# Kernel tuning notes

Hardware: AMD Instinct MI355X
Metric: run time of the kernel (lower is better)

The kernel has to match this reference:

```python
import jax, jax.numpy as jnp
import numpy as np
from jax import lax

POST_NMS_TOP_N = 1000   # cfg[cfg_key].RPN_POST_NMS_TOP_N
NMS_THRESH = 0.7        # cfg[cfg_key].RPN_NMS_THRESH
NEG = -1e9
B, N = 4, 65536


def setup_inputs() -> dict:
    key = jax.random.key(0)
    k0, k1, k2, k3, k4, k5, k6 = jax.random.split(key, 7)
    scores = jax.random.uniform(k0, (B, N), dtype=jnp.float32)
    # small deltas so exp(dw) stays in a realistic range
    bbox_deltas = 0.1 * jax.random.normal(k1, (B, N, 4), dtype=jnp.float32)
    # plausible anchor boxes inside a 1024x1024 image
    cx = jax.random.uniform(k2, (N,), minval=0.0, maxval=1024.0)
    cy = jax.random.uniform(k3, (N,), minval=0.0, maxval=1024.0)
    w = jax.random.uniform(k4, (N,), minval=16.0, maxval=256.0)
    h = jax.random.uniform(k5, (N,), minval=16.0, maxval=256.0)
    anchors = jnp.stack([cx - 0.5 * w, cy - 0.5 * h, cx + 0.5 * w, cy + 0.5 * h], axis=-1).astype(jnp.float32)
    im_info = jnp.tile(jnp.array([[1024.0, 1024.0, 1.0]], dtype=jnp.float32), (B, 1))
    ids = jax.random.randint(k6, (N,), 0, 5, dtype=jnp.int32)  # FPN level ids
    return {"scores": scores, "bbox_deltas": bbox_deltas, "anchors": anchors,
            "im_info": im_info, "ids": ids}


def _iou_one(box, boxes):
    # box [4], boxes [N,4]; mmcv convention (no +1)
    x1 = jnp.maximum(box[0], boxes[:, 0])
    y1 = jnp.maximum(box[1], boxes[:, 1])
    x2 = jnp.minimum(box[2], boxes[:, 2])
    y2 = jnp.minimum(box[3], boxes[:, 3])
    inter = jnp.clip(x2 - x1, 0.0) * jnp.clip(y2 - y1, 0.0)
    a1 = (box[2] - box[0]) * (box[3] - box[1])
    a2 = (boxes[:, 2] - boxes[:, 0]) * (boxes[:, 3] - boxes[:, 1])
    return inter / jnp.maximum(a1 + a2 - inter, 1e-6)


def _nms_single(boxes, scores, ids):
    # batched_nms: offset boxes by level id so levels never suppress each other
    max_c = jnp.max(boxes) + 1.0
    boxes_off = boxes + (ids.astype(boxes.dtype) * max_c)[:, None]

    def step(s, _):
        i = jnp.argmax(s)
        valid = s[i] > NEG * 0.5
        iou = _iou_one(boxes_off[i], boxes_off)
        s_new = jnp.where(iou > NMS_THRESH, NEG, s).at[i].set(NEG)
        sel = jnp.where(valid, boxes[i], jnp.zeros((4,), boxes.dtype))
        return s_new, sel

    _, sel = lax.scan(step, scores, None, length=POST_NMS_TOP_N)
    return sel  # [POST_NMS_TOP_N, 4], in descending score order (as batched_nms returns)


def _forward(scores, bbox_deltas, anchors, im_info, ids):
    ws = anchors[:, 2] - anchors[:, 0] + 1.0          # [N]
    hs = anchors[:, 3] - anchors[:, 1] + 1.0
    ctr_x = anchors[:, 0] + 0.5 * ws
    ctr_y = anchors[:, 1] + 0.5 * hs
    dx, dy, dw, dh = (bbox_deltas[..., 0], bbox_deltas[..., 1],
                      bbox_deltas[..., 2], bbox_deltas[..., 3])  # [B,N]
    pcx = dx * ws + ctr_x
    pcy = dy * hs + ctr_y
    pw = jnp.exp(dw) * ws
    ph = jnp.exp(dh) * hs
    proposals = jnp.stack([pcx - 0.5 * pw, pcy - 0.5 * ph,
                           pcx + 0.5 * pw, pcy + 0.5 * ph], axis=-1)  # [B,N,4]
    # clip_boxes: x in [0, w-1], y in [0, h-1]
    wmax = im_info[:, 1][:, None] - 1.0
    hmax = im_info[:, 0][:, None] - 1.0
    x1 = jnp.clip(proposals[..., 0], 0.0, wmax)
    y1 = jnp.clip(proposals[..., 1], 0.0, hmax)
    x2 = jnp.clip(proposals[..., 2], 0.0, wmax)
    y2 = jnp.clip(proposals[..., 3], 0.0, hmax)
    proposals = jnp.stack([x1, y1, x2, y2], axis=-1)
    # per-image batched NMS (greedy descending-score selection == sort + NMS)
    sel = jax.vmap(_nms_single, in_axes=(0, 0, None))(proposals, scores, ids)  # [B,topN,4]
    batch_col = jnp.broadcast_to(
        jnp.arange(scores.shape[0], dtype=sel.dtype)[:, None, None],
        (scores.shape[0], POST_NMS_TOP_N, 1))
    return jnp.concatenate([batch_col, sel], axis=-1)  # [B,topN,5]


def reference(scores, bbox_deltas, anchors, im_info, ids):
    return _forward(scores, bbox_deltas, anchors, im_info, ids)
```

## Files before the change

kernel.cpp:

```cpp
#include <hip/hip_runtime.h>
#include <stdint.h>

#define NB     65536
#define BATCH  4
#define TOPN   1000
#define MMAX   2048
#define NTILE  (MMAX / 64)
#define NPAIRS (NTILE * (NTILE + 1) / 2)
#define CAP    128
#define KSUP   8
#define UNC    128
#define THRESH 0.974f
#define NEGV   (-1e9f)
#define NMS_T  0.7f

#define OFF_CBLK   64
#define OFF_MBLK   1088
#define OFF_KRAW   2112
#define OFF_SBOX   264256
#define OFF_SLEV   395328
#define OFF_CNT2   428096
#define OFF_SUP    460864

__device__ __forceinline__ void decode_box(const float4* __restrict__ anchors4,
                                           const float4* __restrict__ deltas4,
                                           int b, int i, float wmax, float hmax,
                                           float& x1, float& y1, float& x2, float& y2) {
  float4 a = anchors4[i];
  float4 d = deltas4[(size_t)b * NB + i];
  float ws = a.z - a.x + 1.0f;
  float hs = a.w - a.y + 1.0f;
  float cx = a.x + 0.5f * ws;
  float cy = a.y + 0.5f * hs;
  float pcx = d.x * ws + cx;
  float pcy = d.y * hs + cy;
  float pw = expf(d.z) * ws;
  float ph = expf(d.w) * hs;
  x1 = pcx - 0.5f * pw; y1 = pcy - 0.5f * ph;
  x2 = pcx + 0.5f * pw; y2 = pcy + 0.5f * ph;
  x1 = fminf(fmaxf(x1, 0.0f), wmax);
  y1 = fminf(fmaxf(y1, 0.0f), hmax);
  x2 = fminf(fmaxf(x2, 0.0f), wmax);
  y2 = fminf(fmaxf(y2, 0.0f), hmax);
}

__device__ __forceinline__ uint32_t blockscan(uint32_t v, volatile uint32_t* wsum,
                                              int tid, uint32_t* total) {
  __syncthreads();
  int lane = tid & 63, wid = tid >> 6;
  uint32_t x = v;
  for (int off = 1; off < 64; off <<= 1) {
    uint32_t u = __shfl_up(x, off, 64);
    if (lane >= off) x += u;
  }
  if (lane == 63) wsum[wid] = x;
  __syncthreads();
  if (tid == 0) {
    uint32_t run = 0;
    for (int w = 0; w < 4; ++w) { uint32_t t = wsum[w]; wsum[w] = run; run += t; }
    wsum[4] = run;
  }
  __syncthreads();
  *total = wsum[4];
  return x - v + wsum[wid];
}

__global__ __launch_bounds__(256) void k_prep(const float* __restrict__ scores,
                                              const float4* __restrict__ deltas4,
                                              const float4* __restrict__ anchors4,
                                              const float* __restrict__ im_info,
                                              unsigned long long* __restrict__ keys_raw,
                                              uint32_t* __restrict__ cnt_blk,
                                              uint32_t* __restrict__ maxc_blk) {
  const int b = blockIdx.x >> 6;
  const int blk = blockIdx.x & 63;
  const int tid = threadIdx.x;
  const int lane = tid & 63, wid = tid >> 6;
  __shared__ uint32_t wsum[5];
  __shared__ float fred[4];
  const float wmax = im_info[b * 3 + 1] - 1.0f;
  const float hmax = im_info[b * 3 + 0] - 1.0f;
  float sc4[4];
  uint32_t cmask = 0, ccount = 0;
  float mcoord = 0.0f;
#pragma unroll
  for (int k = 0; k < 4; ++k) {
    int i = (blk << 10) + (k << 8) + tid;
    float x1, y1, x2, y2;
    decode_box(anchors4, deltas4, b, i, wmax, hmax, x1, y1, x2, y2);
    mcoord = fmaxf(mcoord, fmaxf(fmaxf(x1, y1), fmaxf(x2, y2)));
    float sc = scores[(size_t)b * NB + i];
    sc4[k] = sc;
    if (sc >= THRESH) { cmask |= (1u << k); ccount++; }
  }
  for (int o = 32; o > 0; o >>= 1) mcoord = fmaxf(mcoord, __shfl_xor(mcoord, o, 64));
  if (lane == 0) fred[wid] = mcoord;
  uint32_t total;
  uint32_t ebase = blockscan(ccount, wsum, tid, &total);
  if (tid == 0) {
    cnt_blk[blockIdx.x] = total;
    maxc_blk[blockIdx.x] =
        __float_as_uint(fmaxf(fmaxf(fred[0], fred[1]), fmaxf(fred[2], fred[3])));
  }
  uint32_t p = ebase;
  unsigned long long* dst = keys_raw + (size_t)blockIdx.x * CAP;
#pragma unroll
  for (int k = 0; k < 4; ++k) {
    if (cmask & (1u << k)) {
      if (p < (uint32_t)CAP) {
        int i = (blk << 10) + (k << 8) + tid;
        dst[p] = ((unsigned long long)(~__float_as_uint(sc4[k])) << 32) | (uint32_t)i;
      }
      p++;
    }
  }
}

__global__ __launch_bounds__(256) void k_rank(const uint32_t* __restrict__ cnt_blk,
                                              const uint32_t* __restrict__ maxc_blk,
                                              const unsigned long long* __restrict__ keys_raw,
                                              const float4* __restrict__ deltas4,
                                              const float4* __restrict__ anchors4,
                                              const float* __restrict__ im_info,
                                              const int* __restrict__ ids,
                                              uint32_t* ctrs,
                                              float4* sboxes, int* slev,
                                              uint32_t* cnt2) {
  const int b = blockIdx.y;
  const int r = blockIdx.x;
  const int tid = threadIdx.x;
  const int lane = tid & 63, wid = tid >> 6;
  __shared__ unsigned long long sk[MMAX];
  __shared__ uint32_t scnt[64], sbs[64];
  __shared__ uint32_t psum[256];
  __shared__ uint32_t meta[3];

  if (tid < 64) {
    uint32_t c = cnt_blk[b * 64 + tid];
    uint32_t cc = min(c, (uint32_t)CAP);
    uint32_t mb = maxc_blk[b * 64 + tid];
    scnt[tid] = cc;
    uint32_t x = cc;
    for (int off = 1; off < 64; off <<= 1) {
      uint32_t u = __shfl_up(x, off, 64);
      if (lane >= off) x += u;
    }
    sbs[tid] = x - cc;
    for (int off = 32; off > 0; off >>= 1)
      mb = max(mb, (uint32_t)__shfl_xor((int)mb, off, 64));
    unsigned long long ov = __ballot(c > (uint32_t)CAP);
    if (tid == 63) { meta[0] = x; meta[2] = (ov != 0ULL) ? 1u : 0u; }
    if (tid == 0) meta[1] = mb;
  }
  __syncthreads();
  uint32_t nsum = meta[0];
  int n = min((int)nsum, MMAX);
  uint32_t flag = meta[2] | ((nsum > (uint32_t)MMAX) ? 1u : 0u);
  if (r == 0 && tid == 0) {
    ctrs[b] = (uint32_t)n;
    ctrs[4 + b] = meta[1];
    ctrs[8 + b] = flag;
  }
  if (tid < 64) cnt2[(size_t)b * MMAX + r * 64 + tid] = 0u;
  {
    int k = tid >> 2, q = tid & 3;
    uint32_t cb = sbs[k], cc = scnt[k];
    const unsigned long long* src = keys_raw + ((size_t)b * 64 + k) * CAP;
    for (uint32_t o = q; o < cc; o += 4) {
      uint32_t d = cb + o;
      if (d < (uint32_t)MMAX) sk[d] = src[o];
    }
  }
  for (int i = tid; i < MMAX; i += 256) if (i >= n) sk[i] = ~0ULL;
  __syncthreads();
  int c = r * 64 + lane;
  uint32_t partial = 0;
  if (c < n) {
    unsigned long long myk = sk[c];
    const ulonglong2* p2 = (const ulonglong2*)(sk + (size_t)wid * 512);
    for (int it = 0; it < 256; it += 4) {
      ulonglong2 a = p2[it], bq = p2[it + 1], cq = p2[it + 2], dq = p2[it + 3];
      partial += (uint32_t)(a.x < myk) + (uint32_t)(a.y < myk) +
                 (uint32_t)(bq.x < myk) + (uint32_t)(bq.y < myk) +
                 (uint32_t)(cq.x < myk) + (uint32_t)(cq.y < myk) +
                 (uint32_t)(dq.x < myk) + (uint32_t)(dq.y < myk);
    }
  }
  psum[wid * 64 + lane] = partial;
  __syncthreads();
  if (tid < 64) {
    int cc = r * 64 + tid;
    if (cc < n) {
      uint32_t rank = psum[tid] + psum[64 + tid] + psum[128 + tid] + psum[192 + tid];
      if (rank < (uint32_t)MMAX) {
        unsigned long long key = sk[cc];
        int i = (int)(uint32_t)key;
        float wmax = im_info[b * 3 + 1] - 1.0f;
        float hmax = im_info[b * 3 + 0] - 1.0f;
        float x1, y1, x2, y2;
        decode_box(anchors4, deltas4, b, i, wmax, hmax, x1, y1, x2, y2);
        sboxes[(size_t)b * MMAX + rank] = make_float4(x1, y1, x2, y2);
        slev[(size_t)b * MMAX + rank] = ids[i];
      }
    }
  }
}

__global__ __launch_bounds__(64) void k_pairs(uint32_t* ctrs,
                                              const float4* __restrict__ sboxes,
                                              const int* __restrict__ slev,
                                              uint32_t* cnt2, int* suplist) {
  int b = blockIdx.y;
  int p = blockIdx.x;
  int tj = (int)((sqrtf(8.0f * (float)p + 1.0f) - 1.0f) * 0.5f);
  while ((tj + 1) * (tj + 2) / 2 <= p) ++tj;
  while (tj * (tj + 1) / 2 > p) --tj;
  int ti = p - tj * (tj + 1) / 2;
  int n = min((int)ctrs[b], MMAX);
  if (tj * 64 >= n) return;
  float max_c = __uint_as_float(ctrs[4 + b]) + 1.0f;
  int lane = threadIdx.x;

  __shared__ float4 ib[64];
  __shared__ int il[64];
  int ii = ti * 64 + lane;
  if (ii < n) {
    float4 v = sboxes[(size_t)b * MMAX + ii];
    int lv = slev[(size_t)b * MMAX + ii];
    float off = (float)lv * max_c;
    ib[lane] = make_float4(v.x + off, v.y + off, v.z + off, v.w + off);
    il[lane] = lv;
  } else {
    il[lane] = -1;
  }
  int j = tj * 64 + lane;
  float4 J = make_float4(0.f, 0.f, 0.f, 0.f);
  int jl = -2;
  float aj = 0.0f;
  if (j < n) {
    float4 v = sboxes[(size_t)b * MMAX + j];
    jl = slev[(size_t)b * MMAX + j];
    float off = (float)jl * max_c;
    J = make_float4(v.x + off, v.y + off, v.z + off, v.w + off);
    aj = (J.z - J.x) * (J.w - J.y);
  }
  __syncthreads();
  if (j < n) {
    int imax = (ti == tj) ? lane : 64;
    for (int k = 0; k < imax; ++k) {
      if (il[k] != jl) continue;
      float4 I = ib[k];
      float xx1 = fmaxf(I.x, J.x), yy1 = fmaxf(I.y, J.y);
      float xx2 = fminf(I.z, J.z), yy2 = fminf(I.w, J.w);
      float inter = fmaxf(xx2 - xx1, 0.0f) * fmaxf(yy2 - yy1, 0.0f);
      float ai = (I.z - I.x) * (I.w - I.y);
      float iou = inter / fmaxf((ai + aj) - inter, 1e-6f);
      if (iou > NMS_T) {
        uint32_t s = atomicAdd(&cnt2[(size_t)b * MMAX + j], 1u);
        if (s < (uint32_t)KSUP) suplist[((size_t)b * MMAX + j) * KSUP + s] = ti * 64 + k;
        else ctrs[8 + b] = 1u;
      }
    }
  }
}

__device__ __forceinline__ uint32_t scan_pair(uint32_t pairsum, volatile uint32_t* wsum,
                                              int tid, uint32_t* total_out) {
  int lane = tid & 63, wid = tid >> 6;
  uint32_t v = pairsum;
  for (int off = 1; off < 64; off <<= 1) {
    uint32_t u = __shfl_up(v, off, 64);
    if (lane >= off) v += u;
  }
  if (lane == 63) wsum[wid] = v;
  __syncthreads();
  if (tid == 0) {
    uint32_t run = 0;
    for (int w = 0; w < 16; ++w) { uint32_t t = wsum[w]; wsum[w] = run; run += t; }
    wsum[16] = run;
  }
  __syncthreads();
  uint32_t incl = v + wsum[wid];
  *total_out = wsum[16];
  return incl - pairsum;
}

__global__ __launch_bounds__(1024) void k_resolve(uint32_t* ctrs,
                                                  const uint32_t* __restrict__ cnt2,
                                                  const int* __restrict__ suplist,
                                                  const float4* __restrict__ sboxes,
                                                  float* __restrict__ out) {
  int b = blockIdx.x;
  int tid = threadIdx.x;
  __shared__ uint8_t kept[MMAX];
  __shared__ uint32_t wsum[17];
  __shared__ uint16_t unc[UNC];
  __shared__ int supld[UNC][KSUP];
  __shared__ uint8_t supn[UNC];
  int n = min((int)ctrs[b], MMAX);
  int j0 = tid * 2, j1 = tid * 2 + 1;
  uint32_t c0 = (j0 < n) ? cnt2[(size_t)b * MMAX + j0] : 0u;
  uint32_t c1 = (j1 < n) ? cnt2[(size_t)b * MMAX + j1] : 0u;
  kept[j0] = (j0 < n && c0 == 0u) ? 1 : 0;
  kept[j1] = (j1 < n && c1 == 0u) ? 1 : 0;
  uint32_t u0 = (j0 < n && c0 > 0u) ? 1u : 0u;
  uint32_t u1 = (j1 < n && c1 > 0u) ? 1u : 0u;
  uint32_t tot_unc;
  uint32_t base = scan_pair(u0 + u1, wsum, tid, &tot_unc);
  if (u0) {
    uint32_t p = base;
    if (p < UNC) {
      int m = (int)min(c0, (uint32_t)KSUP);
      unc[p] = (uint16_t)j0; supn[p] = (uint8_t)m;
      for (int s = 0; s < m; ++s) supld[p][s] = suplist[((size_t)b * MMAX + j0) * KSUP + s];
    }
  }
  if (u1) {
    uint32_t p = base + u0;
    if (p < UNC) {
      int m = (int)min(c1, (uint32_t)KSUP);
      unc[p] = (uint16_t)j1; supn[p] = (uint8_t)m;
      for (int s = 0; s < m; ++s) supld[p][s] = suplist[((size_t)b * MMAX + j1) * KSUP + s];
    }
  }
  __syncthreads();
  if (tid < 64) {
    int nu = (int)min(tot_unc, (uint32_t)UNC);
    for (int u = 0; u < nu; ++u) {
      int m = (int)supn[u];
      int pred = (tid < m) ? (int)kept[supld[u][tid]] : 0;
      unsigned long long bal = __ballot(pred);
      if (tid == 0) kept[unc[u]] = (bal == 0ULL) ? 1 : 0;
    }
  }
  __syncthreads();
  uint32_t k0 = kept[j0], k1 = kept[j1];
  uint32_t total;
  uint32_t pbase = scan_pair(k0 + k1, wsum, tid, &total);
  if (k0 && pbase < (uint32_t)TOPN) {
    float4 bx = sboxes[(size_t)b * MMAX + j0];
    size_t o = ((size_t)b * TOPN + pbase) * 5;
    out[o] = (float)b; out[o+1] = bx.x; out[o+2] = bx.y; out[o+3] = bx.z; out[o+4] = bx.w;
  }
  if (k1) {
    uint32_t p = pbase + k0;
    if (p < (uint32_t)TOPN) {
      float4 bx = sboxes[(size_t)b * MMAX + j1];
      size_t o = ((size_t)b * TOPN + p) * 5;
      out[o] = (float)b; out[o+1] = bx.x; out[o+2] = bx.y; out[o+3] = bx.z; out[o+4] = bx.w;
    }
  }
  for (int t = tid; t < TOPN; t += 1024) {
    if ((uint32_t)t >= total) {
      size_t o = ((size_t)b * TOPN + t) * 5;
      out[o] = (float)b; out[o+1] = 0.0f; out[o+2] = 0.0f; out[o+3] = 0.0f; out[o+4] = 0.0f;
    }
  }
  if (tid == 0 && (total < (uint32_t)TOPN || tot_unc > (uint32_t)UNC)) ctrs[8 + b] = 1u;
}

__global__ __launch_bounds__(1024) void k_fallback(const float* __restrict__ scores,
                                                   const float4* __restrict__ deltas4,
                                                   const float4* __restrict__ anchors4,
                                                   const float* __restrict__ im_info,
                                                   const int* __restrict__ ids,
                                                   const uint32_t* __restrict__ ctrs,
                                                   float* __restrict__ out) {
  int b = blockIdx.x;
  if (ctrs[8 + b] == 0u) return;
  int tid = threadIdx.x;
  __shared__ uint32_t mask[NB / 32];
  __shared__ float rv[1024];
  __shared__ int ri[1024];
  float max_c = __uint_as_float(ctrs[4 + b]) + 1.0f;
  float wmax = im_info[b * 3 + 1] - 1.0f;
  float hmax = im_info[b * 3 + 0] - 1.0f;
  for (int i = tid; i < NB / 32; i += 1024) mask[i] = 0u;
  __syncthreads();
  for (int it = 0; it < TOPN; ++it) {
    float bv = -3e38f; int bi = 0x7fffffff;
    for (int i = tid; i < NB; i += 1024) {
      bool sup = (mask[i >> 5] >> (i & 31)) & 1u;
      float v = sup ? NEGV : scores[(size_t)b * NB + i];
      if (v > bv || (v == bv && i < bi)) { bv = v; bi = i; }
    }
    rv[tid] = bv; ri[tid] = bi;
    __syncthreads();
    for (int s = 512; s > 0; s >>= 1) {
      if (tid < s) {
        float v2 = rv[tid + s]; int i2 = ri[tid + s];
        if (v2 > rv[tid] || (v2 == rv[tid] && i2 < ri[tid])) { rv[tid] = v2; ri[tid] = i2; }
      }
      __syncthreads();
    }
    int ii = ri[0]; float vv = rv[0];
    bool valid = vv > NEGV * 0.5f;
    if (!valid) {
      if (tid == 0) {
        size_t o = ((size_t)b * TOPN + it) * 5;
        out[o] = (float)b; out[o+1] = 0; out[o+2] = 0; out[o+3] = 0; out[o+4] = 0;
      }
      __syncthreads();
      continue;
    }
    float x1, y1, x2, y2;
    decode_box(anchors4, deltas4, b, ii, wmax, hmax, x1, y1, x2, y2);
    int lv = ids[ii];
    float off = (float)lv * max_c;
    float s0 = x1 + off, s1 = y1 + off, s2 = x2 + off, s3 = y2 + off;
    float a1 = (s2 - s0) * (s3 - s1);
    if (tid == 0) {
      size_t o = ((size_t)b * TOPN + it) * 5;
      out[o] = (float)b; out[o+1] = x1; out[o+2] = y1; out[o+3] = x2; out[o+4] = y2;
    }
    for (int j = tid; j < NB; j += 1024) {
      if ((mask[j >> 5] >> (j & 31)) & 1u) continue;
      if (ids[j] != lv) continue;
      float bx1, by1, bx2, by2;
      decode_box(anchors4, deltas4, b, j, wmax, hmax, bx1, by1, bx2, by2);
      float t0 = bx1 + off, t1 = by1 + off, t2 = bx2 + off, t3 = by2 + off;
      float xx1 = fmaxf(s0, t0), yy1 = fmaxf(s1, t1);
      float xx2 = fminf(s2, t2), yy2 = fminf(s3, t3);
      float inter = fmaxf(xx2 - xx1, 0.0f) * fmaxf(yy2 - yy1, 0.0f);
      float a2r = (t2 - t0) * (t3 - t1);
      float iou = inter / fmaxf(a1 + a2r - inter, 1e-6f);
      if (iou > NMS_T) atomicOr(&mask[j >> 5], 1u << (j & 31));
    }
    if (tid == 0) atomicOr(&mask[ii >> 5], 1u << (ii & 31));
    __syncthreads();
  }
}

extern "C" void kernel_launch(void* const* d_in, const int* in_sizes, int n_in,
                              void* d_out, int out_size, void* d_ws, size_t ws_size,
                              hipStream_t stream) {
  const float*  scores   = (const float*)d_in[0];
  const float4* deltas4  = (const float4*)d_in[1];
  const float4* anchors4 = (const float4*)d_in[2];
  const float*  im_info  = (const float*)d_in[3];
  const int*    ids      = (const int*)d_in[4];
  float* out = (float*)d_out;

  char* ws = (char*)d_ws;
  uint32_t*           ctrs     = (uint32_t*)ws;
  uint32_t*           cnt_blk  = (uint32_t*)(ws + OFF_CBLK);
  uint32_t*           maxc_blk = (uint32_t*)(ws + OFF_MBLK);
  unsigned long long* keys_raw = (unsigned long long*)(ws + OFF_KRAW);
  float4*             sboxes   = (float4*)(ws + OFF_SBOX);
  int*                slev     = (int*)(ws + OFF_SLEV);
  uint32_t*           cnt2     = (uint32_t*)(ws + OFF_CNT2);
  int*                suplist  = (int*)(ws + OFF_SUP);

  hipLaunchKernelGGL(k_prep, dim3(64 * BATCH), dim3(256), 0, stream,
                     scores, deltas4, anchors4, im_info, keys_raw, cnt_blk, maxc_blk);
  hipLaunchKernelGGL(k_rank, dim3(NTILE, BATCH), dim3(256), 0, stream,
                     cnt_blk, maxc_blk, keys_raw, deltas4, anchors4, im_info, ids,
                     ctrs, sboxes, slev, cnt2);
  hipLaunchKernelGGL(k_pairs, dim3(NPAIRS, BATCH), dim3(64), 0, stream,
                     ctrs, sboxes, slev, cnt2, suplist);
  hipLaunchKernelGGL(k_resolve, dim3(BATCH), dim3(1024), 0, stream,
                     ctrs, cnt2, suplist, sboxes, out);
  hipLaunchKernelGGL(k_fallback, dim3(BATCH), dim3(1024), 0, stream,
                     scores, deltas4, anchors4, im_info, ids, ctrs, out);
}
```

Baseline: 102.7 us.

## Drop full-box decode from prep and fold fallback into output kernel

The prep kernel now reads only scores, as float4 loads, to build candidate keys. It no longer decodes every anchor box just to find the maximum coordinate, which avoids streaming all deltas and anchors on the common path. Level separation in the pair kernel now relies on the level-id comparison instead of coordinate offsets, so the global max coordinate is only needed by the exact fallback, which computes it lazily. The resolve and fallback kernels are merged into one, removing a launch; the merged kernel carries a larger shared-memory footprint and does an extra decode pass when the fallback fires.

```diff
diff --git a/kernel.cpp b/kernel.cpp
--- a/kernel.cpp
+++ b/kernel.cpp
@@ -15,12 +15,11 @@
 #define NMS_T  0.7f
 
 #define OFF_CBLK   64
-#define OFF_MBLK   1088
-#define OFF_KRAW   2112
-#define OFF_SBOX   264256
-#define OFF_SLEV   395328
-#define OFF_CNT2   428096
-#define OFF_SUP    460864
+#define OFF_KRAW   1088
+#define OFF_SBOX   263232
+#define OFF_SLEV   394304
+#define OFF_CNT2   427072
+#define OFF_SUP    459840
 
 __device__ __forceinline__ void decode_box(const float4* __restrict__ anchors4,
                                            const float4* __restrict__ deltas4,
@@ -66,49 +65,28 @@
 }
 
 __global__ __launch_bounds__(256) void k_prep(const float* __restrict__ scores,
-                                              const float4* __restrict__ deltas4,
-                                              const float4* __restrict__ anchors4,
-                                              const float* __restrict__ im_info,
                                               unsigned long long* __restrict__ keys_raw,
-                                              uint32_t* __restrict__ cnt_blk,
-                                              uint32_t* __restrict__ maxc_blk) {
+                                              uint32_t* __restrict__ cnt_blk) {
   const int b = blockIdx.x >> 6;
   const int blk = blockIdx.x & 63;
   const int tid = threadIdx.x;
-  const int lane = tid & 63, wid = tid >> 6;
   __shared__ uint32_t wsum[5];
-  __shared__ float fred[4];
-  const float wmax = im_info[b * 3 + 1] - 1.0f;
-  const float hmax = im_info[b * 3 + 0] - 1.0f;
-  float sc4[4];
+  const float4* s4 = (const float4*)scores + (size_t)b * (NB / 4) + (size_t)blk * 256 + tid;
+  float4 s = *s4;
+  float sc4[4] = {s.x, s.y, s.z, s.w};
   uint32_t cmask = 0, ccount = 0;
-  float mcoord = 0.0f;
 #pragma unroll
-  for (int k = 0; k < 4; ++k) {
-    int i = (blk << 10) + (k << 8) + tid;
-    float x1, y1, x2, y2;
-    decode_box(anchors4, deltas4, b, i, wmax, hmax, x1, y1, x2, y2);
-    mcoord = fmaxf(mcoord, fmaxf(fmaxf(x1, y1), fmaxf(x2, y2)));
-    float sc = scores[(size_t)b * NB + i];
-    sc4[k] = sc;
-    if (sc >= THRESH) { cmask |= (1u << k); ccount++; }
-  }
-  for (int o = 32; o > 0; o >>= 1) mcoord = fmaxf(mcoord, __shfl_xor(mcoord, o, 64));
-  if (lane == 0) fred[wid] = mcoord;
+  for (int k = 0; k < 4; ++k)
+    if (sc4[k] >= THRESH) { cmask |= (1u << k); ccount++; }
   uint32_t total;
-  uint32_t ebase = blockscan(ccount, wsum, tid, &total);
-  if (tid == 0) {
-    cnt_blk[blockIdx.x] = total;
-    maxc_blk[blockIdx.x] =
-        __float_as_uint(fmaxf(fmaxf(fred[0], fred[1]), fmaxf(fred[2], fred[3])));
-  }
-  uint32_t p = ebase;
+  uint32_t p = blockscan(ccount, wsum, tid, &total);
+  if (tid == 0) cnt_blk[blockIdx.x] = total;
   unsigned long long* dst = keys_raw + (size_t)blockIdx.x * CAP;
 #pragma unroll
   for (int k = 0; k < 4; ++k) {
     if (cmask & (1u << k)) {
       if (p < (uint32_t)CAP) {
-        int i = (blk << 10) + (k << 8) + tid;
+        int i = (blk << 10) + (tid << 2) + k;
         dst[p] = ((unsigned long long)(~__float_as_uint(sc4[k])) << 32) | (uint32_t)i;
       }
       p++;
@@ -117,7 +95,6 @@
 }
 
 __global__ __launch_bounds__(256) void k_rank(const uint32_t* __restrict__ cnt_blk,
-                                              const uint32_t* __restrict__ maxc_blk,
                                               const unsigned long long* __restrict__ keys_raw,
                                               const float4* __restrict__ deltas4,
                                               const float4* __restrict__ anchors4,
@@ -133,12 +110,11 @@
   __shared__ unsigned long long sk[MMAX];
   __shared__ uint32_t scnt[64], sbs[64];
   __shared__ uint32_t psum[256];
-  __shared__ uint32_t meta[3];
+  __shared__ uint32_t meta[2];
 
   if (tid < 64) {
     uint32_t c = cnt_blk[b * 64 + tid];
     uint32_t cc = min(c, (uint32_t)CAP);
-    uint32_t mb = maxc_blk[b * 64 + tid];
     scnt[tid] = cc;
     uint32_t x = cc;
     for (int off = 1; off < 64; off <<= 1) {
@@ -146,19 +122,15 @@
       if (lane >= off) x += u;
     }
     sbs[tid] = x - cc;
-    for (int off = 32; off > 0; off >>= 1)
-      mb = max(mb, (uint32_t)__shfl_xor((int)mb, off, 64));
     unsigned long long ov = __ballot(c > (uint32_t)CAP);
-    if (tid == 63) { meta[0] = x; meta[2] = (ov != 0ULL) ? 1u : 0u; }
-    if (tid == 0) meta[1] = mb;
+    if (tid == 63) { meta[0] = x; meta[1] = (ov != 0ULL) ? 1u : 0u; }
   }
   __syncthreads();
   uint32_t nsum = meta[0];
   int n = min((int)nsum, MMAX);
-  uint32_t flag = meta[2] | ((nsum > (uint32_t)MMAX) ? 1u : 0u);
+  uint32_t flag = meta[1] | ((nsum > (uint32_t)MMAX) ? 1u : 0u);
   if (r == 0 && tid == 0) {
     ctrs[b] = (uint32_t)n;
-    ctrs[4 + b] = meta[1];
     ctrs[8 + b] = flag;
   }
   if (tid < 64) cnt2[(size_t)b * MMAX + r * 64 + tid] = 0u;
@@ -218,18 +190,14 @@
   int ti = p - tj * (tj + 1) / 2;
   int n = min((int)ctrs[b], MMAX);
   if (tj * 64 >= n) return;
-  float max_c = __uint_as_float(ctrs[4 + b]) + 1.0f;
   int lane = threadIdx.x;
 
   __shared__ float4 ib[64];
   __shared__ int il[64];
   int ii = ti * 64 + lane;
   if (ii < n) {
-    float4 v = sboxes[(size_t)b * MMAX + ii];
-    int lv = slev[(size_t)b * MMAX + ii];
-    float off = (float)lv * max_c;
-    ib[lane] = make_float4(v.x + off, v.y + off, v.z + off, v.w + off);
-    il[lane] = lv;
+    ib[lane] = sboxes[(size_t)b * MMAX + ii];
+    il[lane] = slev[(size_t)b * MMAX + ii];
   } else {
     il[lane] = -1;
   }
@@ -238,10 +206,8 @@
   int jl = -2;
   float aj = 0.0f;
   if (j < n) {
-    float4 v = sboxes[(size_t)b * MMAX + j];
+    J = sboxes[(size_t)b * MMAX + j];
     jl = slev[(size_t)b * MMAX + j];
-    float off = (float)jl * max_c;
-    J = make_float4(v.x + off, v.y + off, v.z + off, v.w + off);
     aj = (J.z - J.x) * (J.w - J.y);
   }
   __syncthreads();
@@ -285,11 +251,16 @@
   return incl - pairsum;
 }
 
-__global__ __launch_bounds__(1024) void k_resolve(uint32_t* ctrs,
-                                                  const uint32_t* __restrict__ cnt2,
-                                                  const int* __restrict__ suplist,
-                                                  const float4* __restrict__ sboxes,
-                                                  float* __restrict__ out) {
+__global__ __launch_bounds__(1024) void k_out(const float* __restrict__ scores,
+                                              const float4* __restrict__ deltas4,
+                                              const float4* __restrict__ anchors4,
+                                              const float* __restrict__ im_info,
+                                              const int* __restrict__ ids,
+                                              const uint32_t* __restrict__ ctrs,
+                                              const uint32_t* __restrict__ cnt2,
+                                              const int* __restrict__ suplist,
+                                              const float4* __restrict__ sboxes,
+                                              float* __restrict__ out) {
   int b = blockIdx.x;
   int tid = threadIdx.x;
   __shared__ uint8_t kept[MMAX];
@@ -356,27 +327,34 @@
       out[o] = (float)b; out[o+1] = 0.0f; out[o+2] = 0.0f; out[o+3] = 0.0f; out[o+4] = 0.0f;
     }
   }
-  if (tid == 0 && (total < (uint32_t)TOPN || tot_unc > (uint32_t)UNC)) ctrs[8 + b] = 1u;
-}
-
-__global__ __launch_bounds__(1024) void k_fallback(const float* __restrict__ scores,
-                                                   const float4* __restrict__ deltas4,
-                                                   const float4* __restrict__ anchors4,
-                                                   const float* __restrict__ im_info,
-                                                   const int* __restrict__ ids,
-                                                   const uint32_t* __restrict__ ctrs,
-                                                   float* __restrict__ out) {
-  int b = blockIdx.x;
-  if (ctrs[8 + b] == 0u) return;
-  int tid = threadIdx.x;
+
+  bool needFB = (ctrs[8 + b] != 0u) || (total < (uint32_t)TOPN) || (tot_unc > (uint32_t)UNC);
+  if (!needFB) return;
+
   __shared__ uint32_t mask[NB / 32];
   __shared__ float rv[1024];
   __shared__ int ri[1024];
-  float max_c = __uint_as_float(ctrs[4 + b]) + 1.0f;
-  float wmax = im_info[b * 3 + 1] - 1.0f;
-  float hmax = im_info[b * 3 + 0] - 1.0f;
+  __shared__ float fm[16];
+  const float wmax = im_info[b * 3 + 1] - 1.0f;
+  const float hmax = im_info[b * 3 + 0] - 1.0f;
+  __syncthreads();
+  float mx = 0.0f;
+  for (int i = tid; i < NB; i += 1024) {
+    float x1, y1, x2, y2;
+    decode_box(anchors4, deltas4, b, i, wmax, hmax, x1, y1, x2, y2);
+    mx = fmaxf(mx, fmaxf(fmaxf(x1, y1), fmaxf(x2, y2)));
+  }
+  for (int o = 32; o > 0; o >>= 1) mx = fmaxf(mx, __shfl_xor(mx, o, 64));
+  if ((tid & 63) == 0) fm[tid >> 6] = mx;
+  __syncthreads();
+  if (tid == 0) {
+    float m = fm[0];
+    for (int w = 1; w < 16; ++w) m = fmaxf(m, fm[w]);
+    fm[0] = m;
+  }
   for (int i = tid; i < NB / 32; i += 1024) mask[i] = 0u;
   __syncthreads();
+  float max_c = fm[0] + 1.0f;
   for (int it = 0; it < TOPN; ++it) {
     float bv = -3e38f; int bi = 0x7fffffff;
     for (int i = tid; i < NB; i += 1024) {
@@ -444,7 +422,6 @@
   char* ws = (char*)d_ws;
   uint32_t*           ctrs     = (uint32_t*)ws;
   uint32_t*           cnt_blk  = (uint32_t*)(ws + OFF_CBLK);
-  uint32_t*           maxc_blk = (uint32_t*)(ws + OFF_MBLK);
   unsigned long long* keys_raw = (unsigned long long*)(ws + OFF_KRAW);
   float4*             sboxes   = (float4*)(ws + OFF_SBOX);
   int*                slev     = (int*)(ws + OFF_SLEV);
@@ -452,14 +429,13 @@
   int*                suplist  = (int*)(ws + OFF_SUP);
 
   hipLaunchKernelGGL(k_prep, dim3(64 * BATCH), dim3(256), 0, stream,
-                     scores, deltas4, anchors4, im_info, keys_raw, cnt_blk, maxc_blk);
+                     scores, keys_raw, cnt_blk);
   hipLaunchKernelGGL(k_rank, dim3(NTILE, BATCH), dim3(256), 0, stream,
-                     cnt_blk, maxc_blk, keys_raw, deltas4, anchors4, im_info, ids,
+                     cnt_blk, keys_raw, deltas4, anchors4, im_info, ids,
                      ctrs, sboxes, slev, cnt2);
   hipLaunchKernelGGL(k_pairs, dim3(NPAIRS, BATCH), dim3(64), 0, stream,
                      ctrs, sboxes, slev, cnt2, suplist);
-  hipLaunchKernelGGL(k_resolve, dim3(BATCH), dim3(1024), 0, stream,
-                     ctrs, cnt2, suplist, sboxes, out);
-  hipLaunchKernelGGL(k_fallback, dim3(BATCH), dim3(1024), 0, stream,
-                     scores, deltas4, anchors4, im_info, ids, ctrs, out);
-}
+  hipLaunchKernelGGL(k_out, dim3(BATCH), dim3(1024), 0, stream,
+                     scores, deltas4, anchors4, im_info, ids, ctrs, cnt2, suplist,
+                     sboxes, out);
+}
```

Measured after the change: 101.0 us (median of 2 runs). Within noise of the previous version (-1.6%).
